# Kernel tuning notes

Hardware: AMD Instinct MI355X
Metric: run time of the kernel (lower is better)

The kernel has to match this reference:

```python
import jax, jax.numpy as jnp
import numpy as np
import math

D_MODEL = 1024
N_HEAD = 16
D_K = D_MODEL // N_HEAD  # 64
SEQ = 1024
BATCH = 8


def setup_inputs() -> dict:
    k = jax.random.key(0)
    ks = jax.random.split(k, 11)
    f32 = jnp.float32
    scale = 1.0 / math.sqrt(D_MODEL)
    return {
        "query": jax.random.normal(ks[0], (BATCH, SEQ, D_MODEL), dtype=f32),
        "key": jax.random.normal(ks[1], (BATCH, SEQ, D_MODEL), dtype=f32),
        "value": jax.random.normal(ks[2], (BATCH, SEQ, D_MODEL), dtype=f32),
        # Shaw-style relative position table a[q_pos, k_pos, d_k]
        "rel": jax.random.normal(ks[3], (SEQ, SEQ, D_K), dtype=f32) * 0.02,
        "W_q": jax.random.normal(ks[4], (D_MODEL, D_MODEL), dtype=f32) * scale,
        "b_q": jnp.zeros((D_MODEL,), dtype=f32),
        "W_k": jax.random.normal(ks[5], (D_MODEL, D_MODEL), dtype=f32) * scale,
        "b_k": jnp.zeros((D_MODEL,), dtype=f32),
        "W_v": jax.random.normal(ks[6], (D_MODEL, D_MODEL), dtype=f32) * scale,
        "b_v": jnp.zeros((D_MODEL,), dtype=f32),
        # boolean mask: True = masked out (matches torch masked_fill semantics)
        "mask": jax.random.randint(ks[7], (BATCH, SEQ, SEQ), 0, 4) == 0,
    }


def reference(query, key, value, rel, W_q, b_q, W_k, b_k, W_v, b_v, mask):
    B, S, D = query.shape
    H, dk = N_HEAD, D // N_HEAD

    def proj(x, W, b):
        # [B,S,D] -> [B,H,S,dk]
        return (x @ W + b).reshape(B, S, H, dk).transpose(0, 2, 1, 3)

    Q = proj(query, W_q, b_q)
    K = proj(key, W_k, b_k)
    V = proj(value, W_v, b_v)

    # E_1 = Q K^T / sqrt(d_k): [B,H,Sq,Sk]
    scores = jnp.einsum("bhqd,bhkd->bhqk", Q, K) / math.sqrt(dk)
    # E_2 = Q x relative_position (per query position), added UNscaled as in source
    scores = scores + jnp.einsum("bhqd,qkd->bhqk", Q, rel)
    # masked_fill(mask, -1e8)
    scores = jnp.where(mask[:, None, :, :], jnp.float32(-1e8), scores)
    attn = jax.nn.softmax(scores, axis=-1)
    out = jnp.einsum("bhqk,bhkd->bhqd", attn, V)  # [B,H,S,dk]
    return out.transpose(0, 2, 1, 3).reshape(B, S, D)
```

## Files before the change

kernel.cpp:

```cpp
#include <hip/hip_runtime.h>

typedef _Float16 h8_t __attribute__((ext_vector_type(8)));
typedef _Float16 h4_t __attribute__((ext_vector_type(4)));
typedef float f4_t __attribute__((ext_vector_type(4)));

#define MFMA16(a, b, c) __builtin_amdgcn_mfma_f32_16x16x32_f16((a), (b), (c), 0, 0, 0)

__device__ inline void gl_lds16(const _Float16* g, _Float16* l) {
    __builtin_amdgcn_global_load_lds(
        (const __attribute__((address_space(1))) unsigned int*)g,
        (__attribute__((address_space(3))) unsigned int*)l, 16, 0, 0);
}

__global__ void cvt4(const float* __restrict__ in, _Float16* __restrict__ out, int n4) {
    int i = blockIdx.x * 256 + threadIdx.x;
    if (i < n4) {
        f4_t v = *(const f4_t*)(in + (size_t)i * 4);
        h4_t h;
        for (int j = 0; j < 4; ++j) h[j] = (_Float16)v[j];
        *(h4_t*)(out + (size_t)i * 4) = h;
    }
}

__global__ void wtrans(const float* __restrict__ W, _Float16* __restrict__ Wt) {
    __shared__ float tile[32][33];
    int tid = threadIdx.x;
    int tx = tid & 31, ty = tid >> 5;
    int nb = blockIdx.x * 32, kb = blockIdx.y * 32;
    for (int p = 0; p < 4; ++p)
        tile[ty + p * 8][tx] = W[(size_t)(kb + ty + p * 8) * 1024 + nb + tx];
    __syncthreads();
    for (int p = 0; p < 4; ++p)
        Wt[(size_t)(nb + ty + p * 8) * 1024 + kb + tx] = (_Float16)tile[tx][ty + p * 8];
}

__global__ __launch_bounds__(256, 2) void proj_gemm(
    const _Float16* __restrict__ X, const _Float16* __restrict__ Wt,
    const float* __restrict__ bias, _Float16* __restrict__ Out,
    float scale, int vmode)
{
    __shared__ __align__(16) _Float16 Asm[128 * 32];
    __shared__ __align__(16) _Float16 Bsm[128 * 32];
    int tid = threadIdx.x;
    int wave = tid >> 6, lane = tid & 63;
    int l15 = lane & 15, quad = lane >> 4;
    int m0 = blockIdx.x * 128, n0 = blockIdx.y * 128;
    int wm = (wave >> 1) * 64, wn = (wave & 1) * 64;
    f4_t acc[4][4] = {};
    int f0 = wave * 128 + lane;

    for (int kt = 0; kt < 1024; kt += 32) {
        for (int j = 0; j < 2; ++j) {
            int f = f0 + j * 64;
            int r = f >> 2, c = (f & 3) * 8;
            gl_lds16(&X[(size_t)(m0 + r) * 1024 + kt + c], &Asm[f * 8]);
            gl_lds16(&Wt[(size_t)(n0 + r) * 1024 + kt + c], &Bsm[f * 8]);
        }
        __syncthreads();
        h8_t af[4], bf[4];
        for (int i = 0; i < 4; ++i) af[i] = *(const h8_t*)&Asm[(wm + i * 16 + l15) * 32 + quad * 8];
        for (int j = 0; j < 4; ++j) bf[j] = *(const h8_t*)&Bsm[(wn + j * 16 + l15) * 32 + quad * 8];
        for (int i = 0; i < 4; ++i)
            for (int j = 0; j < 4; ++j)
                acc[i][j] = MFMA16(af[i], bf[j], acc[i][j]);
        __syncthreads();
    }
    for (int j = 0; j < 4; ++j) {
        int n = n0 + wn + j * 16 + l15;
        float bv = bias[n];
        int h = n >> 6, d = n & 63;
        for (int i = 0; i < 4; ++i) {
            for (int r = 0; r < 4; ++r) {
                int m = m0 + wm + i * 16 + quad * 4 + r;
                int bb = m >> 10, ss = m & 1023;
                float v = (acc[i][j][r] + bv) * scale;
                size_t oidx = vmode ? (((size_t)(bb * 16 + h) * 64 + d) * 1024 + ss)
                                    : (((size_t)(bb * 16 + h) * 1024 + ss) * 64 + d);
                Out[oidx] = (_Float16)v;
            }
        }
    }
}

__device__ inline h8_t ld_rel(const _Float16* relh, const float* relf, size_t idx) {
    if (relh) return *(const h8_t*)(relh + idx);
    f4_t a = *(const f4_t*)(relf + idx);
    f4_t b = *(const f4_t*)(relf + idx + 4);
    h8_t h;
    for (int j = 0; j < 4; ++j) { h[j] = (_Float16)a[j]; h[4 + j] = (_Float16)b[j]; }
    return h;
}

__global__ __launch_bounds__(256, 2) void attn_kernel(
    const _Float16* __restrict__ Qh,
    const _Float16* __restrict__ Kh,
    const _Float16* __restrict__ Vt,
    const _Float16* __restrict__ relh,
    const float* __restrict__ relf,
    const int* __restrict__ mask,
    float* __restrict__ out)
{
    __shared__ __align__(16) _Float16 R_lds[2][16][17][36];
    __shared__ __align__(16) _Float16 P_lds[16][16][40];

    const int tid = threadIdx.x;
    const int wave = tid >> 6, lane = tid & 63;
    const int l15 = lane & 15, quad = lane >> 4;
    const int b = blockIdx.y;
    const int q0 = blockIdx.x * 16;

    h8_t bQ[4][2];
    h8_t bR[4][2];
    for (int gi = 0; gi < 4; ++gi) {
        int g = wave * 4 + gi;
        const _Float16* qp = Qh + ((size_t)(b * 16 + g) * 1024 + q0 + l15) * 64 + quad * 8;
        bQ[gi][0] = *(const h8_t*)qp;
        bQ[gi][1] = *(const h8_t*)(qp + 32);
    }
    for (int qi = 0; qi < 4; ++qi) {
        int q = q0 + wave * 4 + qi;
        const _Float16* qp = Qh + ((size_t)(b * 16 + l15) * 1024 + q) * 64 + quad * 8;
        bR[qi][0] = *(const h8_t*)qp;
        bR[qi][1] = *(const h8_t*)(qp + 32);
    }

    f4_t acc[4][4] = {};
    float mst[4], lst[4];
    for (int gi = 0; gi < 4; ++gi) { mst[gi] = -1e30f; lst[gi] = 0.0f; }

    int buf = 0;
    for (int t0 = 0; t0 < 1024; t0 += 32, buf ^= 1) {
        const int* mrow = &mask[((size_t)b * 1024 + q0 + l15) * 1024 + t0];
        int4 mk0 = *(const int4*)(mrow + quad * 4);
        int4 mk1 = *(const int4*)(mrow + 16 + quad * 4);

        h8_t relv[4][2][2];
        for (int qi = 0; qi < 4; ++qi) {
            size_t rb = ((size_t)(q0 + wave * 4 + qi) * 1024 + t0 + l15) * 64 + quad * 8;
            relv[qi][0][0] = ld_rel(relh, relf, rb);
            relv[qi][0][1] = ld_rel(relh, relf, rb + 32);
            relv[qi][1][0] = ld_rel(relh, relf, rb + 1024);
            relv[qi][1][1] = ld_rel(relh, relf, rb + 1056);
        }
        for (int qi = 0; qi < 4; ++qi) {
            for (int tm = 0; tm < 2; ++tm) {
                f4_t c = {0.f, 0.f, 0.f, 0.f};
                c = MFMA16(relv[qi][tm][0], bR[qi][0], c);
                c = MFMA16(relv[qi][tm][1], bR[qi][1], c);
                h4_t h;
                for (int r = 0; r < 4; ++r) h[r] = (_Float16)c[r];
                *(h4_t*)&R_lds[buf][wave * 4 + qi][l15][tm * 16 + quad * 4] = h;
            }
        }

        h8_t kv[4][2][2];
        for (int gi = 0; gi < 4; ++gi) {
            const _Float16* kp =
                Kh + ((size_t)(b * 16 + wave * 4 + gi) * 1024 + t0 + l15) * 64 + quad * 8;
            kv[gi][0][0] = *(const h8_t*)kp;
            kv[gi][0][1] = *(const h8_t*)(kp + 32);
            kv[gi][1][0] = *(const h8_t*)(kp + 1024);
            kv[gi][1][1] = *(const h8_t*)(kp + 1056);
        }
        __syncthreads();

        int mm[8] = {mk0.x, mk0.y, mk0.z, mk0.w, mk1.x, mk1.y, mk1.z, mk1.w};

        for (int gi = 0; gi < 4; ++gi) {
            int g = wave * 4 + gi;
            f4_t s[2];
            for (int tm = 0; tm < 2; ++tm) {
                h4_t rh = *(const h4_t*)&R_lds[buf][l15][g][tm * 16 + quad * 4];
                f4_t c;
                for (int r = 0; r < 4; ++r) c[r] = (float)rh[r];
                c = MFMA16(kv[gi][tm][0], bQ[gi][0], c);
                c = MFMA16(kv[gi][tm][1], bQ[gi][1], c);
                s[tm] = c;
            }
            for (int tm = 0; tm < 2; ++tm)
                for (int r = 0; r < 4; ++r)
                    if (mm[tm * 4 + r]) s[tm][r] = -1e8f;

            float mx = s[0][0];
            for (int tm = 0; tm < 2; ++tm)
                for (int r = 0; r < 4; ++r) mx = fmaxf(mx, s[tm][r]);
            mx = fmaxf(mx, __shfl_xor(mx, 16));
            mx = fmaxf(mx, __shfl_xor(mx, 32));
            float mnew = fmaxf(mst[gi], mx);
            float alpha = __expf(mst[gi] - mnew);
            mst[gi] = mnew;
            float rs = 0.0f;
            for (int tm = 0; tm < 2; ++tm)
                for (int r = 0; r < 4; ++r) {
                    float p = __expf(s[tm][r] - mnew);
                    s[tm][r] = p;
                    rs += p;
                }
            rs += __shfl_xor(rs, 16);
            rs += __shfl_xor(rs, 32);
            lst[gi] = lst[gi] * alpha + rs;
            for (int dm = 0; dm < 4; ++dm) acc[gi][dm] *= alpha;
            for (int tm = 0; tm < 2; ++tm) {
                h4_t h;
                for (int r = 0; r < 4; ++r) h[r] = (_Float16)s[tm][r];
                *(h4_t*)&P_lds[g][l15][tm * 16 + quad * 4] = h;
            }
        }

        h8_t vv[4][4];
        for (int gi = 0; gi < 4; ++gi) {
            const _Float16* vp =
                Vt + (size_t)(b * 16 + wave * 4 + gi) * 65536 + t0 + quad * 8;
            for (int dm = 0; dm < 4; ++dm)
                vv[gi][dm] = *(const h8_t*)(vp + (size_t)(dm * 16 + l15) * 1024);
        }
        for (int gi = 0; gi < 4; ++gi) {
            h8_t bp = *(const h8_t*)&P_lds[wave * 4 + gi][l15][quad * 8];
            for (int dm = 0; dm < 4; ++dm)
                acc[gi][dm] = MFMA16(vv[gi][dm], bp, acc[gi][dm]);
        }
    }

    for (int gi = 0; gi < 4; ++gi) {
        int g = wave * 4 + gi;
        float linv = 1.0f / lst[gi];
        for (int dm = 0; dm < 4; ++dm) {
            f4_t v = acc[gi][dm] * linv;
            float* op = out + ((size_t)b * 1024 + q0 + l15) * 1024 + g * 64 + dm * 16 + quad * 4;
            *(f4_t*)op = v;
        }
    }
}

extern "C" void kernel_launch(void* const* d_in, const int* in_sizes, int n_in,
                              void* d_out, int out_size, void* d_ws, size_t ws_size,
                              hipStream_t stream) {
    const float* q    = (const float*)d_in[0];
    const float* k    = (const float*)d_in[1];
    const float* v    = (const float*)d_in[2];
    const float* rel  = (const float*)d_in[3];
    const float* Wq   = (const float*)d_in[4];
    const float* bq   = (const float*)d_in[5];
    const float* Wk   = (const float*)d_in[6];
    const float* bk   = (const float*)d_in[7];
    const float* Wv   = (const float*)d_in[8];
    const float* bv   = (const float*)d_in[9];
    const int*   mask = (const int*)d_in[10];
    float* out = (float*)d_out;

    const size_t NEL = 8ull * 1024 * 1024;
    const size_t WEL = 1024ull * 1024;
    const size_t RELE = 1024ull * 1024 * 64;

    char* w = (char*)d_ws;
    size_t off = 0;
    auto alloc = [&](size_t bytes) { char* p = w + off; off += bytes; return p; };
    _Float16* qx  = (_Float16*)alloc(NEL * 2);
    _Float16* kx  = (_Float16*)alloc(NEL * 2);
    _Float16* vx  = (_Float16*)alloc(NEL * 2);
    _Float16* Wqt = (_Float16*)alloc(WEL * 2);
    _Float16* Wkt = (_Float16*)alloc(WEL * 2);
    _Float16* Wvt = (_Float16*)alloc(WEL * 2);
    _Float16* Qh  = (_Float16*)alloc(NEL * 2);
    _Float16* Kh  = (_Float16*)alloc(NEL * 2);
    _Float16* Vth = (_Float16*)alloc(NEL * 2);
    _Float16* relh = nullptr;
    if (ws_size >= off + RELE * 2) relh = (_Float16*)alloc(RELE * 2);

    cvt4<<<(int)(NEL / 4 / 256), 256, 0, stream>>>(q, qx, (int)(NEL / 4));
    cvt4<<<(int)(NEL / 4 / 256), 256, 0, stream>>>(k, kx, (int)(NEL / 4));
    cvt4<<<(int)(NEL / 4 / 256), 256, 0, stream>>>(v, vx, (int)(NEL / 4));
    if (relh)
        cvt4<<<(int)(RELE / 4 / 256), 256, 0, stream>>>(rel, relh, (int)(RELE / 4));

    dim3 tg(32, 32);
    wtrans<<<tg, 256, 0, stream>>>(Wq, Wqt);
    wtrans<<<tg, 256, 0, stream>>>(Wk, Wkt);
    wtrans<<<tg, 256, 0, stream>>>(Wv, Wvt);

    dim3 pg(64, 8);
    proj_gemm<<<pg, 256, 0, stream>>>(qx, Wqt, bq, Qh, 1.0f, 0);
    proj_gemm<<<pg, 256, 0, stream>>>(kx, Wkt, bk, Kh, 0.125f, 0);
    proj_gemm<<<pg, 256, 0, stream>>>(vx, Wvt, bv, Vth, 1.0f, 1);

    dim3 ag(64, 8);
    attn_kernel<<<ag, 256, 0, stream>>>(Qh, Kh, Vth, relh, rel, mask, out);
}
```

Before: 940.0 us.

## Fuse input fp16 conversion into projection GEMM and restructure attention loop

```diff
diff --git a/kernel.cpp b/kernel.cpp
--- a/kernel.cpp
+++ b/kernel.cpp
@@ -35,7 +35,7 @@
 }
 
 __global__ __launch_bounds__(256, 2) void proj_gemm(
-    const _Float16* __restrict__ X, const _Float16* __restrict__ Wt,
+    const float* __restrict__ X, const _Float16* __restrict__ Wt,
     const float* __restrict__ bias, _Float16* __restrict__ Out,
     float scale, int vmode)
 {
@@ -50,26 +50,45 @@
     int f0 = wave * 128 + lane;
 
     for (int kt = 0; kt < 1024; kt += 32) {
+        #pragma unroll
         for (int j = 0; j < 2; ++j) {
             int f = f0 + j * 64;
             int r = f >> 2, c = (f & 3) * 8;
-            gl_lds16(&X[(size_t)(m0 + r) * 1024 + kt + c], &Asm[f * 8]);
             gl_lds16(&Wt[(size_t)(n0 + r) * 1024 + kt + c], &Bsm[f * 8]);
+        }
+        #pragma unroll
+        for (int j = 0; j < 2; ++j) {
+            int f = f0 + j * 64;
+            int r = f >> 2, c = (f & 3) * 8;
+            const float* xp = &X[(size_t)(m0 + r) * 1024 + kt + c];
+            f4_t x0 = *(const f4_t*)xp;
+            f4_t x1 = *(const f4_t*)(xp + 4);
+            h8_t h;
+            #pragma unroll
+            for (int i = 0; i < 4; ++i) { h[i] = (_Float16)x0[i]; h[4 + i] = (_Float16)x1[i]; }
+            *(h8_t*)&Asm[f * 8] = h;
         }
         __syncthreads();
         h8_t af[4], bf[4];
+        #pragma unroll
         for (int i = 0; i < 4; ++i) af[i] = *(const h8_t*)&Asm[(wm + i * 16 + l15) * 32 + quad * 8];
+        #pragma unroll
         for (int j = 0; j < 4; ++j) bf[j] = *(const h8_t*)&Bsm[(wn + j * 16 + l15) * 32 + quad * 8];
+        #pragma unroll
         for (int i = 0; i < 4; ++i)
+            #pragma unroll
             for (int j = 0; j < 4; ++j)
                 acc[i][j] = MFMA16(af[i], bf[j], acc[i][j]);
         __syncthreads();
     }
+    #pragma unroll
     for (int j = 0; j < 4; ++j) {
         int n = n0 + wn + j * 16 + l15;
         float bv = bias[n];
         int h = n >> 6, d = n & 63;
+        #pragma unroll
         for (int i = 0; i < 4; ++i) {
+            #pragma unroll
             for (int r = 0; r < 4; ++r) {
                 int m = m0 + wm + i * 16 + quad * 4 + r;
                 int bb = m >> 10, ss = m & 1023;
@@ -100,8 +119,7 @@
     const int* __restrict__ mask,
     float* __restrict__ out)
 {
-    __shared__ __align__(16) _Float16 R_lds[2][16][17][36];
-    __shared__ __align__(16) _Float16 P_lds[16][16][40];
+    extern __shared__ _Float16 R_lds[];
 
     const int tid = threadIdx.x;
     const int wave = tid >> 6, lane = tid & 63;
@@ -110,120 +128,174 @@
     const int q0 = blockIdx.x * 16;
 
     h8_t bQ[4][2];
-    h8_t bR[4][2];
+    #pragma unroll
     for (int gi = 0; gi < 4; ++gi) {
         int g = wave * 4 + gi;
         const _Float16* qp = Qh + ((size_t)(b * 16 + g) * 1024 + q0 + l15) * 64 + quad * 8;
         bQ[gi][0] = *(const h8_t*)qp;
         bQ[gi][1] = *(const h8_t*)(qp + 32);
     }
-    for (int qi = 0; qi < 4; ++qi) {
-        int q = q0 + wave * 4 + qi;
-        const _Float16* qp = Qh + ((size_t)(b * 16 + l15) * 1024 + q) * 64 + quad * 8;
-        bR[qi][0] = *(const h8_t*)qp;
-        bR[qi][1] = *(const h8_t*)(qp + 32);
-    }
 
     f4_t acc[4][4] = {};
     float mst[4], lst[4];
+    #pragma unroll
     for (int gi = 0; gi < 4; ++gi) { mst[gi] = -1e30f; lst[gi] = 0.0f; }
 
-    int buf = 0;
-    for (int t0 = 0; t0 < 1024; t0 += 32, buf ^= 1) {
-        const int* mrow = &mask[((size_t)b * 1024 + q0 + l15) * 1024 + t0];
-        int4 mk0 = *(const int4*)(mrow + quad * 4);
-        int4 mk1 = *(const int4*)(mrow + 16 + quad * 4);
-
-        h8_t relv[4][2][2];
+    for (int st = 0; st < 8; ++st) {
+        const int t0 = st * 128;
+
+        h8_t bR[4][2];
+        #pragma unroll
         for (int qi = 0; qi < 4; ++qi) {
-            size_t rb = ((size_t)(q0 + wave * 4 + qi) * 1024 + t0 + l15) * 64 + quad * 8;
-            relv[qi][0][0] = ld_rel(relh, relf, rb);
-            relv[qi][0][1] = ld_rel(relh, relf, rb + 32);
-            relv[qi][1][0] = ld_rel(relh, relf, rb + 1024);
-            relv[qi][1][1] = ld_rel(relh, relf, rb + 1056);
-        }
+            const _Float16* qp =
+                Qh + ((size_t)(b * 16 + l15) * 1024 + q0 + wave * 4 + qi) * 64 + quad * 8;
+            bR[qi][0] = *(const h8_t*)qp;
+            bR[qi][1] = *(const h8_t*)(qp + 32);
+        }
+        #pragma unroll
         for (int qi = 0; qi < 4; ++qi) {
-            for (int tm = 0; tm < 2; ++tm) {
-                f4_t c = {0.f, 0.f, 0.f, 0.f};
-                c = MFMA16(relv[qi][tm][0], bR[qi][0], c);
-                c = MFMA16(relv[qi][tm][1], bR[qi][1], c);
-                h4_t h;
-                for (int r = 0; r < 4; ++r) h[r] = (_Float16)c[r];
-                *(h4_t*)&R_lds[buf][wave * 4 + qi][l15][tm * 16 + quad * 4] = h;
-            }
-        }
-
-        h8_t kv[4][2][2];
-        for (int gi = 0; gi < 4; ++gi) {
-            const _Float16* kp =
-                Kh + ((size_t)(b * 16 + wave * 4 + gi) * 1024 + t0 + l15) * 64 + quad * 8;
-            kv[gi][0][0] = *(const h8_t*)kp;
-            kv[gi][0][1] = *(const h8_t*)(kp + 32);
-            kv[gi][1][0] = *(const h8_t*)(kp + 1024);
-            kv[gi][1][1] = *(const h8_t*)(kp + 1056);
+            const int q = q0 + wave * 4 + qi;
+            const int ql = wave * 4 + qi;
+            h8_t rv[4][2][2];
+            #pragma unroll
+            for (int tl = 0; tl < 4; ++tl)
+                #pragma unroll
+                for (int tm = 0; tm < 2; ++tm) {
+                    size_t rb = ((size_t)q * 1024 + t0 + tl * 32 + tm * 16 + l15) * 64 + quad * 8;
+                    rv[tl][tm][0] = ld_rel(relh, relf, rb);
+                    rv[tl][tm][1] = ld_rel(relh, relf, rb + 32);
+                }
+            #pragma unroll
+            for (int tl = 0; tl < 4; ++tl)
+                #pragma unroll
+                for (int tm = 0; tm < 2; ++tm) {
+                    f4_t c = {0.f, 0.f, 0.f, 0.f};
+                    c = MFMA16(rv[tl][tm][0], bR[qi][0], c);
+                    c = MFMA16(rv[tl][tm][1], bR[qi][1], c);
+                    h4_t h;
+                    #pragma unroll
+                    for (int r = 0; r < 4; ++r) h[r] = (_Float16)c[r];
+                    *(h4_t*)&R_lds[((size_t)ql * 17 + l15) * 136 + tl * 32 + tm * 16 + quad * 4] = h;
+                }
         }
         __syncthreads();
 
-        int mm[8] = {mk0.x, mk0.y, mk0.z, mk0.w, mk1.x, mk1.y, mk1.z, mk1.w};
-
-        for (int gi = 0; gi < 4; ++gi) {
-            int g = wave * 4 + gi;
-            f4_t s[2];
-            for (int tm = 0; tm < 2; ++tm) {
-                h4_t rh = *(const h4_t*)&R_lds[buf][l15][g][tm * 16 + quad * 4];
-                f4_t c;
-                for (int r = 0; r < 4; ++r) c[r] = (float)rh[r];
-                c = MFMA16(kv[gi][tm][0], bQ[gi][0], c);
-                c = MFMA16(kv[gi][tm][1], bQ[gi][1], c);
-                s[tm] = c;
-            }
-            for (int tm = 0; tm < 2; ++tm)
-                for (int r = 0; r < 4; ++r)
-                    if (mm[tm * 4 + r]) s[tm][r] = -1e8f;
-
-            float mx = s[0][0];
-            for (int tm = 0; tm < 2; ++tm)
-                for (int r = 0; r < 4; ++r) mx = fmaxf(mx, s[tm][r]);
-            mx = fmaxf(mx, __shfl_xor(mx, 16));
-            mx = fmaxf(mx, __shfl_xor(mx, 32));
-            float mnew = fmaxf(mst[gi], mx);
-            float alpha = __expf(mst[gi] - mnew);
-            mst[gi] = mnew;
-            float rs = 0.0f;
-            for (int tm = 0; tm < 2; ++tm)
+        #pragma unroll
+        for (int tt = 0; tt < 4; ++tt) {
+            const int t = t0 + tt * 32;
+
+            const int* mrow = &mask[((size_t)b * 1024 + q0 + l15) * 1024 + t];
+            int4 mk0 = *(const int4*)(mrow + quad * 4);
+            int4 mk1 = *(const int4*)(mrow + 16 + quad * 4);
+
+            h8_t kv[4][2][2];
+            #pragma unroll
+            for (int gi = 0; gi < 4; ++gi) {
+                const _Float16* kp =
+                    Kh + ((size_t)(b * 16 + wave * 4 + gi) * 1024 + t + l15) * 64 + quad * 8;
+                kv[gi][0][0] = *(const h8_t*)kp;
+                kv[gi][0][1] = *(const h8_t*)(kp + 32);
+                kv[gi][1][0] = *(const h8_t*)(kp + 1024);
+                kv[gi][1][1] = *(const h8_t*)(kp + 1056);
+            }
+
+            f4_t s[4][2];
+            #pragma unroll
+            for (int gi = 0; gi < 4; ++gi) {
+                const int g = wave * 4 + gi;
+                #pragma unroll
+                for (int tm = 0; tm < 2; ++tm) {
+                    h4_t rh = *(const h4_t*)&R_lds[((size_t)l15 * 17 + g) * 136 + tt * 32 + tm * 16 + quad * 4];
+                    f4_t c;
+                    #pragma unroll
+                    for (int r = 0; r < 4; ++r) c[r] = (float)rh[r];
+                    c = MFMA16(kv[gi][tm][0], bQ[gi][0], c);
+                    c = MFMA16(kv[gi][tm][1], bQ[gi][1], c);
+                    s[gi][tm] = c;
+                }
+            }
+
+            h8_t vv[4][4];
+            #pragma unroll
+            for (int gi = 0; gi < 4; ++gi) {
+                const _Float16* vp =
+                    Vt + (size_t)(b * 16 + wave * 4 + gi) * 65536 + t + quad * 8;
+                #pragma unroll
+                for (int dm = 0; dm < 4; ++dm)
+                    vv[gi][dm] = *(const h8_t*)(vp + (size_t)(dm * 16 + l15) * 1024);
+            }
+
+            int mm[8] = {mk0.x, mk0.y, mk0.z, mk0.w, mk1.x, mk1.y, mk1.z, mk1.w};
+
+            h8_t bp[4];
+            #pragma unroll
+            for (int gi = 0; gi < 4; ++gi) {
+                #pragma unroll
+                for (int tm = 0; tm < 2; ++tm)
+                    #pragma unroll
+                    for (int r = 0; r < 4; ++r)
+                        if (mm[tm * 4 + r]) s[gi][tm][r] = -1e8f;
+
+                float mx = s[gi][0][0];
+                #pragma unroll
+                for (int tm = 0; tm < 2; ++tm)
+                    #pragma unroll
+                    for (int r = 0; r < 4; ++r) mx = fmaxf(mx, s[gi][tm][r]);
+                mx = fmaxf(mx, __shfl_xor(mx, 16));
+                mx = fmaxf(mx, __shfl_xor(mx, 32));
+                float mnew = fmaxf(mst[gi], mx);
+                float alpha = __expf(mst[gi] - mnew);
+                mst[gi] = mnew;
+                float rs = 0.0f;
+                #pragma unroll
+                for (int tm = 0; tm < 2; ++tm)
+                    #pragma unroll
+                    for (int r = 0; r < 4; ++r) {
+                        float p = __expf(s[gi][tm][r] - mnew);
+                        s[gi][tm][r] = p;
+                        rs += p;
+                    }
+                rs += __shfl_xor(rs, 16);
+                rs += __shfl_xor(rs, 32);
+                lst[gi] = lst[gi] * alpha + rs;
+                #pragma unroll
+                for (int dm = 0; dm < 4; ++dm) acc[gi][dm] *= alpha;
+
+                union { h4_t h; unsigned u[2]; } pk0, pk1;
+                #pragma unroll
                 for (int r = 0; r < 4; ++r) {
-                    float p = __expf(s[tm][r] - mnew);
-                    s[tm][r] = p;
-                    rs += p;
+                    pk0.h[r] = (_Float16)s[gi][0][r];
+                    pk1.h[r] = (_Float16)s[gi][1][r];
                 }
-            rs += __shfl_xor(rs, 16);
-            rs += __shfl_xor(rs, 32);
-            lst[gi] = lst[gi] * alpha + rs;
-            for (int dm = 0; dm < 4; ++dm) acc[gi][dm] *= alpha;
-            for (int tm = 0; tm < 2; ++tm) {
-                h4_t h;
-                for (int r = 0; r < 4; ++r) h[r] = (_Float16)s[tm][r];
-                *(h4_t*)&P_lds[g][l15][tm * 16 + quad * 4] = h;
-            }
-        }
-
-        h8_t vv[4][4];
-        for (int gi = 0; gi < 4; ++gi) {
-            const _Float16* vp =
-                Vt + (size_t)(b * 16 + wave * 4 + gi) * 65536 + t0 + quad * 8;
-            for (int dm = 0; dm < 4; ++dm)
-                vv[gi][dm] = *(const h8_t*)(vp + (size_t)(dm * 16 + l15) * 1024);
-        }
-        for (int gi = 0; gi < 4; ++gi) {
-            h8_t bp = *(const h8_t*)&P_lds[wave * 4 + gi][l15][quad * 8];
-            for (int dm = 0; dm < 4; ++dm)
-                acc[gi][dm] = MFMA16(vv[gi][dm], bp, acc[gi][dm]);
-        }
-    }
-
+                const int src0 = ((quad & 1) << 5) + l15;
+                const int src1 = src0 + 16;
+                unsigned a0 = __shfl(pk0.u[0], src0), a1 = __shfl(pk0.u[1], src0);
+                unsigned c0 = __shfl(pk1.u[0], src0), c1 = __shfl(pk1.u[1], src0);
+                unsigned d0 = __shfl(pk0.u[0], src1), d1 = __shfl(pk0.u[1], src1);
+                unsigned e0 = __shfl(pk1.u[0], src1), e1 = __shfl(pk1.u[1], src1);
+                const bool hi2 = quad >= 2;
+                union { h8_t h; unsigned u[4]; } r8;
+                r8.u[0] = hi2 ? c0 : a0;
+                r8.u[1] = hi2 ? c1 : a1;
+                r8.u[2] = hi2 ? e0 : d0;
+                r8.u[3] = hi2 ? e1 : d1;
+                bp[gi] = r8.h;
+            }
+
+            #pragma unroll
+            for (int gi = 0; gi < 4; ++gi)
+                #pragma unroll
+                for (int dm = 0; dm < 4; ++dm)
+                    acc[gi][dm] = MFMA16(vv[gi][dm], bp[gi], acc[gi][dm]);
+        }
+        __syncthreads();
+    }
+
+    #pragma unroll
     for (int gi = 0; gi < 4; ++gi) {
         int g = wave * 4 + gi;
         float linv = 1.0f / lst[gi];
+        #pragma unroll
         for (int dm = 0; dm < 4; ++dm) {
             f4_t v = acc[gi][dm] * linv;
             float* op = out + ((size_t)b * 1024 + q0 + l15) * 1024 + g * 64 + dm * 16 + quad * 4;
@@ -255,9 +327,6 @@
     char* w = (char*)d_ws;
     size_t off = 0;
     auto alloc = [&](size_t bytes) { char* p = w + off; off += bytes; return p; };
-    _Float16* qx  = (_Float16*)alloc(NEL * 2);
-    _Float16* kx  = (_Float16*)alloc(NEL * 2);
-    _Float16* vx  = (_Float16*)alloc(NEL * 2);
     _Float16* Wqt = (_Float16*)alloc(WEL * 2);
     _Float16* Wkt = (_Float16*)alloc(WEL * 2);
     _Float16* Wvt = (_Float16*)alloc(WEL * 2);
@@ -267,9 +336,6 @@
     _Float16* relh = nullptr;
     if (ws_size >= off + RELE * 2) relh = (_Float16*)alloc(RELE * 2);
 
-    cvt4<<<(int)(NEL / 4 / 256), 256, 0, stream>>>(q, qx, (int)(NEL / 4));
-    cvt4<<<(int)(NEL / 4 / 256), 256, 0, stream>>>(k, kx, (int)(NEL / 4));
-    cvt4<<<(int)(NEL / 4 / 256), 256, 0, stream>>>(v, vx, (int)(NEL / 4));
     if (relh)
         cvt4<<<(int)(RELE / 4 / 256), 256, 0, stream>>>(rel, relh, (int)(RELE / 4));
 
@@ -279,10 +345,11 @@
     wtrans<<<tg, 256, 0, stream>>>(Wv, Wvt);
 
     dim3 pg(64, 8);
-    proj_gemm<<<pg, 256, 0, stream>>>(qx, Wqt, bq, Qh, 1.0f, 0);
-    proj_gemm<<<pg, 256, 0, stream>>>(kx, Wkt, bk, Kh, 0.125f, 0);
-    proj_gemm<<<pg, 256, 0, stream>>>(vx, Wvt, bv, Vth, 1.0f, 1);
+    proj_gemm<<<pg, 256, 0, stream>>>(q, Wqt, bq, Qh, 1.0f, 0);
+    proj_gemm<<<pg, 256, 0, stream>>>(k, Wkt, bk, Kh, 0.125f, 0);
+    proj_gemm<<<pg, 256, 0, stream>>>(v, Wvt, bv, Vth, 1.0f, 1);
 
     dim3 ag(64, 8);
-    attn_kernel<<<ag, 256, 0, stream>>>(Qh, Kh, Vth, relh, rel, mask, out);
-}
+    size_t shb = (size_t)16 * 17 * 136 * sizeof(_Float16);
+    attn_kernel<<<ag, 256, shb, stream>>>(Qh, Kh, Vth, relh, rel, mask, out);
+}
```

After: 1.085 ms. 15.4% more time.
